# Performance work log

Hardware: AMD Instinct MI355X
Metric: run time of the kernel (lower is better)

## Reference

```python
import jax, jax.numpy as jnp
import numpy as np

D = 1024      # embed_size
H = 16        # num_heads
NEXP = 8      # num_experts
TOPK = 3
THRESH = 0.05
COEF = 0.01
B, SQ, SKV = 4, 1024, 1024


def _ln(x, g, b, eps=1e-5):
    m = jnp.mean(x, axis=-1, keepdims=True)
    v = jnp.mean(jnp.square(x - m), axis=-1, keepdims=True)
    return (x - m) * jax.lax.rsqrt(v + eps) * g + b


def setup_inputs() -> dict:
    key = jax.random.key(0)
    ks = jax.random.split(key, 20)
    s = 0.02
    w = lambda k, shape: (jax.random.normal(k, shape, jnp.float32) * s)
    return {
        'query': jax.random.normal(ks[0], (B, SQ, D), jnp.float32),
        'key_value': jax.random.normal(ks[1], (B, SKV, D), jnp.float32),
        'Wq': w(ks[2], (D, D)), 'bq': jnp.zeros((D,), jnp.float32),
        'Wk': w(ks[3], (D, D)), 'bk': jnp.zeros((D,), jnp.float32),
        'Wv': w(ks[4], (D, D)), 'bv': jnp.zeros((D,), jnp.float32),
        'W_in': w(ks[5], (3 * D, D)), 'b_in': jnp.zeros((3 * D,), jnp.float32),
        'W_out': w(ks[6], (D, D)), 'b_out': jnp.zeros((D,), jnp.float32),
        'Wa': w(ks[7], (D, D)), 'ba': jnp.zeros((D,), jnp.float32),
        'ln1_g': jnp.ones((D,), jnp.float32), 'ln1_b': jnp.zeros((D,), jnp.float32),
        'Wg': w(ks[8], (D, NEXP)),
        'ew1': w(ks[9], (NEXP, D, 4 * D)), 'eb1': jnp.zeros((NEXP, 4 * D), jnp.float32),
        'ew2': w(ks[10], (NEXP, 4 * D, D)), 'eb2': jnp.zeros((NEXP, D), jnp.float32),
        'ln2_g': jnp.ones((D,), jnp.float32), 'ln2_b': jnp.zeros((D,), jnp.float32),
    }


def reference(query, key_value, Wq, bq, Wk, bk, Wv, bv, W_in, b_in, W_out, b_out,
              Wa, ba, ln1_g, ln1_b, Wg, ew1, eb1, ew2, eb2, ln2_g, ln2_b):
    Bq, Sq, _ = query.shape
    Skv = key_value.shape[1]
    Dh = D // H
    # outer Q/K/V linears (torch Linear: x @ W.T + b)
    q = query @ Wq.T + bq
    k = key_value @ Wk.T + bk
    v = key_value @ Wv.T + bv
    # nn.MultiheadAttention in-projection
    Wiq, Wik, Wiv = jnp.split(W_in, 3, axis=0)
    biq, bik, biv = jnp.split(b_in, 3)
    qh = (q @ Wiq.T + biq).reshape(Bq, Sq, H, Dh).transpose(0, 2, 1, 3)
    kh = (k @ Wik.T + bik).reshape(Bq, Skv, H, Dh).transpose(0, 2, 1, 3)
    vh = (v @ Wiv.T + biv).reshape(Bq, Skv, H, Dh).transpose(0, 2, 1, 3)
    scores = jnp.einsum('bhqd,bhkd->bhqk', qh, kh) / jnp.sqrt(jnp.float32(Dh))
    attn = jax.nn.softmax(scores, axis=-1)
    o = jnp.einsum('bhqk,bhkd->bhqd', attn, vh).transpose(0, 2, 1, 3).reshape(Bq, Sq, D)
    o = o @ W_out.T + b_out
    # adapt + residual + first_norm
    x = _ln(o @ Wa.T + ba + query, ln1_g, ln1_b)
    # ---- MoE: top-3 softmax gating, threshold on non-top-1 gates ----
    probs = jax.nn.softmax(x @ Wg, axis=-1)                 # [B,S,E]
    topv, topi = jax.lax.top_k(probs, TOPK)                  # [B,S,3]
    keep = jnp.concatenate([jnp.ones_like(topv[..., :1], bool),
                            topv[..., 1:] >= THRESH], axis=-1)
    topv = jnp.where(keep, topv, 0.0)
    combine = jnp.sum(jax.nn.one_hot(topi, NEXP, dtype=x.dtype) * topv[..., None], axis=-2)  # [B,S,E]
    moe_out = jnp.zeros_like(x)
    for e in range(NEXP):  # small fixed expert count
        h = jax.nn.gelu(x @ ew1[e] + eb1[e], approximate=False)
        moe_out = moe_out + combine[..., e:e + 1] * (h @ ew2[e] + eb2[e])
    # load-balance aux loss: E * sum(frac_routed * mean_prob) * coef
    fe = jnp.mean((combine > 0).astype(x.dtype), axis=(0, 1))
    me = jnp.mean(probs, axis=(0, 1))
    aux = COEF * NEXP * jnp.sum(fe * me)
    out = _ln(moe_out + x, ln2_g, ln2_b)
    return out, aux
```

## Files before the change

kernel.cpp:

```cpp
#include <hip/hip_runtime.h>
#include <math.h>

#define THRESH_C 0.05f
#define COEF_C   0.01f

typedef __bf16 bf16;
typedef __bf16 bf16x8 __attribute__((ext_vector_type(8)));
typedef __bf16 bf16x4 __attribute__((ext_vector_type(4)));
typedef float  f32x4  __attribute__((ext_vector_type(4)));

__device__ __forceinline__ void ld16(void* lds_base, const void* g) {
    __builtin_amdgcn_global_load_lds(
        (const __attribute__((address_space(1))) void*)g,
        (__attribute__((address_space(3))) void*)lds_base,
        16, 0, 0);
}

__device__ __forceinline__ int xcd_swz(int orig, int nwg) {
    int q = nwg >> 3, r = nwg & 7;
    int xcd = orig & 7, idx = orig >> 3;
    return (xcd < r ? xcd * (q + 1) : r * (q + 1) + (xcd - r) * q) + idx;
}

__global__ __launch_bounds__(256) void k_f32_to_split(const float* __restrict__ in,
                                                      bf16* __restrict__ hi,
                                                      bf16* __restrict__ lo, long n) {
    long i = ((long)blockIdx.x * 256 + threadIdx.x) * 4;
    if (i >= n) return;
    float4 v = *(const float4*)(in + i);
    bf16x4 h, l;
    h[0] = (bf16)v.x; l[0] = (bf16)(v.x - (float)h[0]);
    h[1] = (bf16)v.y; l[1] = (bf16)(v.y - (float)h[1]);
    h[2] = (bf16)v.z; l[2] = (bf16)(v.z - (float)h[2]);
    h[3] = (bf16)v.w; l[3] = (bf16)(v.w - (float)h[3]);
    *(bf16x4*)(hi + i) = h;
    *(bf16x4*)(lo + i) = l;
}

__global__ __launch_bounds__(256) void k_transpose4_split(const float* __restrict__ w0,
                                                          const float* __restrict__ w1,
                                                          const float* __restrict__ w2,
                                                          const float* __restrict__ w3,
                                                          bf16* __restrict__ oh,
                                                          bf16* __restrict__ ol) {
    __shared__ float t[64][65];
    int z = blockIdx.z;
    const float* in = (z == 0) ? w0 : (z == 1) ? w1 : (z == 2) ? w2 : w3;
    bf16* ohz = oh + (long)z * 1048576;
    bf16* olz = ol + (long)z * 1048576;
    int r0 = blockIdx.y * 64, c0 = blockIdx.x * 64;
    for (int i = threadIdx.x; i < 4096; i += 256) {
        int r = i >> 6, c = i & 63;
        t[r][c] = in[(long)(r0 + r) * 1024 + (c0 + c)];
    }
    __syncthreads();
    for (int i = threadIdx.x; i < 4096; i += 256) {
        int c = i >> 6, r = i & 63;
        float v = t[r][c];
        bf16 h = (bf16)v;
        long o = (long)(c0 + c) * 1024 + (r0 + r);
        ohz[o] = h;
        olz[o] = (bf16)(v - (float)h);
    }
}

__global__ __launch_bounds__(256) void k_transpose_ew(const float* __restrict__ in,
                                                      bf16* __restrict__ out,
                                                      int R, int C) {
    __shared__ bf16 t[64][65];
    const float* ib = in + (long)blockIdx.z * R * C;
    bf16* ob = out + (long)blockIdx.z * R * C;
    int r0 = blockIdx.y * 64, c0 = blockIdx.x * 64;
    for (int i = threadIdx.x; i < 4096; i += 256) {
        int r = i >> 6, c = i & 63;
        t[r][c] = (bf16)ib[(long)(r0 + r) * C + (c0 + c)];
    }
    __syncthreads();
    for (int i = threadIdx.x; i < 4096; i += 256) {
        int c = i >> 6, r = i & 63;
        ob[(long)(c0 + c) * R + (r0 + r)] = t[r][c];
    }
}

__global__ __launch_bounds__(256) void k_bias_fold4(const float* __restrict__ W_in,
                                                    const float* __restrict__ Wa,
                                                    const float* __restrict__ bq,
                                                    const float* __restrict__ bk,
                                                    const float* __restrict__ bv,
                                                    const float* __restrict__ b_out,
                                                    const float* __restrict__ b_in,
                                                    const float* __restrict__ ba,
                                                    float* __restrict__ y) {
    int z = blockIdx.y;
    const float* W  = (z < 3) ? (W_in + (long)z * 1048576) : Wa;
    const float* b1 = (z == 0) ? bq : (z == 1) ? bk : (z == 2) ? bv : b_out;
    const float* b2 = (z < 3) ? (b_in + z * 1024) : ba;
    int row = blockIdx.x * 4 + (threadIdx.x >> 6);
    int lane = threadIdx.x & 63;
    const float* wr = W + (long)row * 1024;
    float s = 0.f;
    for (int k = lane; k < 1024; k += 64) s += wr[k] * b1[k];
#pragma unroll
    for (int o = 32; o >= 1; o >>= 1) s += __shfl_xor(s, o);
    if (lane == 0) y[z * 1024 + row] = b2[row] + s;
}

enum { HP_SPLIT = 0, HP_F32 = 1, HP_SPLIT_HEADS = 2 };

template<int MODE>
__global__ __launch_bounds__(256)
void gemm_hp(const bf16* __restrict__ Ah, const bf16* __restrict__ Al, int lda, long sAz,
             const bf16* __restrict__ Bh, const bf16* __restrict__ Bl, int ldb, long sBz,
             void* __restrict__ Chv, bf16* __restrict__ Cl, int ldc, long sCz,
             const float* __restrict__ bias, long sbz, float alpha, int M, int N, int K) {
    __shared__ alignas(16) bf16 sAh[128 * 32];
    __shared__ alignas(16) bf16 sAl[128 * 32];
    __shared__ alignas(16) bf16 sBh[128 * 32];
    __shared__ alignas(16) bf16 sBl[128 * 32];
    const int bm = blockIdx.y, bn = blockIdx.x, z = blockIdx.z;
    const int tid  = threadIdx.x;
    const int lane = tid & 63, wave = tid >> 6;
    const int quad = lane >> 4, l16 = lane & 15;
    const int wr = wave >> 1, wc = wave & 1;
    const int sr = tid >> 2;
    const int sc = (tid & 3) * 8;

    int arow0 = min(bm * 128 + sr, M - 1);
    int arow1 = min(bm * 128 + sr + 64, M - 1);
    int brow0 = min(bn * 128 + sr, N - 1);
    int brow1 = min(bn * 128 + sr + 64, N - 1);

    const bf16* pAh0 = Ah + (long)z * sAz + (long)arow0 * lda + sc;
    const bf16* pAh1 = Ah + (long)z * sAz + (long)arow1 * lda + sc;
    const bf16* pAl0 = Al + (long)z * sAz + (long)arow0 * lda + sc;
    const bf16* pAl1 = Al + (long)z * sAz + (long)arow1 * lda + sc;
    const bf16* pBh0 = Bh + (long)z * sBz + (long)brow0 * ldb + sc;
    const bf16* pBh1 = Bh + (long)z * sBz + (long)brow1 * ldb + sc;
    const bf16* pBl0 = Bl + (long)z * sBz + (long)brow0 * ldb + sc;
    const bf16* pBl1 = Bl + (long)z * sBz + (long)brow1 * ldb + sc;
    const int wo = wave << 9;

    f32x4 acc[4][4];
#pragma unroll
    for (int i = 0; i < 4; i++)
#pragma unroll
        for (int j = 0; j < 4; j++) acc[i][j] = (f32x4){0.f, 0.f, 0.f, 0.f};

    ld16(sAh + wo,        pAh0);
    ld16(sAh + 2048 + wo, pAh1);
    ld16(sAl + wo,        pAl0);
    ld16(sAl + 2048 + wo, pAl1);
    ld16(sBh + wo,        pBh0);
    ld16(sBh + 2048 + wo, pBh1);
    ld16(sBl + wo,        pBl0);
    ld16(sBl + 2048 + wo, pBl1);
    __syncthreads();

    for (int k0 = 0; k0 < K; k0 += 32) {
        bf16x8 ah[4], al[4], bh[4], bl[4];
#pragma unroll
        for (int i = 0; i < 4; i++) {
            int ro = (wr * 64 + i * 16 + l16) * 32 + quad * 8;
            ah[i] = *(const bf16x8*)&sAh[ro];
            al[i] = *(const bf16x8*)&sAl[ro];
        }
#pragma unroll
        for (int j = 0; j < 4; j++) {
            int ro = (wc * 64 + j * 16 + l16) * 32 + quad * 8;
            bh[j] = *(const bf16x8*)&sBh[ro];
            bl[j] = *(const bf16x8*)&sBl[ro];
        }
        __syncthreads();
        int kn = k0 + 32;
        if (kn < K) {
            ld16(sAh + wo,        pAh0 + kn);
            ld16(sAh + 2048 + wo, pAh1 + kn);
            ld16(sAl + wo,        pAl0 + kn);
            ld16(sAl + 2048 + wo, pAl1 + kn);
            ld16(sBh + wo,        pBh0 + kn);
            ld16(sBh + 2048 + wo, pBh1 + kn);
            ld16(sBl + wo,        pBl0 + kn);
            ld16(sBl + 2048 + wo, pBl1 + kn);
        }
#pragma unroll
        for (int i = 0; i < 4; i++)
#pragma unroll
            for (int j = 0; j < 4; j++) {
                acc[i][j] = __builtin_amdgcn_mfma_f32_16x16x32_bf16(al[i], bh[j], acc[i][j], 0, 0, 0);
                acc[i][j] = __builtin_amdgcn_mfma_f32_16x16x32_bf16(ah[i], bl[j], acc[i][j], 0, 0, 0);
                acc[i][j] = __builtin_amdgcn_mfma_f32_16x16x32_bf16(ah[i], bh[j], acc[i][j], 0, 0, 0);
            }
        __syncthreads();
    }

#pragma unroll
    for (int i = 0; i < 4; i++) {
        int mbase = bm * 128 + wr * 64 + i * 16 + quad * 4;
#pragma unroll
        for (int j = 0; j < 4; j++) {
            int n = bn * 128 + wc * 64 + j * 16 + l16;
            if (n < N) {
                float bv = bias ? bias[(long)z * sbz + n] : 0.f;
#pragma unroll
                for (int r = 0; r < 4; r++) {
                    int m = mbase + r;
                    if (m < M) {
                        float v = alpha * acc[i][j][r] + bv;
                        if (MODE == HP_SPLIT) {
                            long cidx = (long)z * sCz + (long)m * ldc + n;
                            bf16 h = (bf16)v;
                            ((bf16*)Chv)[cidx] = h;
                            Cl[cidx] = (bf16)(v - (float)h);
                        } else if (MODE == HP_F32) {
                            long cidx = (long)z * sCz + (long)m * ldc + n;
                            ((float*)Chv)[cidx] = v;
                        } else {
                            int slice = ((m >> 10) << 4) + (n >> 6);
                            long idx = (long)z * sCz + (long)slice * 65536 + (long)(m & 1023) * 64 + (n & 63);
                            bf16 h = (bf16)v;
                            ((bf16*)Chv)[idx] = h;
                            Cl[idx] = (bf16)(v - (float)h);
                        }
                    }
                }
            }
        }
    }
}

__global__ __launch_bounds__(256)
void gemm_pv(const bf16* __restrict__ Ph, const bf16* __restrict__ Pl,
             const bf16* __restrict__ Vh, const bf16* __restrict__ Vl,
             bf16* __restrict__ Oh, bf16* __restrict__ Ol) {
    __shared__ alignas(16) bf16 sAh[2][128 * 32];
    __shared__ alignas(16) bf16 sAl[2][128 * 32];
    __shared__ alignas(16) bf16 sBh[2][64 * 32];
    __shared__ alignas(16) bf16 sBl[2][64 * 32];
    const int bm = blockIdx.x, z = blockIdx.y;
    const int tid = threadIdx.x, lane = tid & 63, wave = tid >> 6;
    const int quad = lane >> 4, l16 = lane & 15;
    const int wr = wave & 1, wc = wave >> 1;
    const int sr = tid >> 2, sc = (tid & 3) * 8;

    const bf16* pA0h = Ph + (long)z * 1048576 + (long)(bm * 128 + sr) * 1024 + sc;
    const bf16* pA1h = pA0h + 64 * 1024;
    const bf16* pA0l = Pl + (long)z * 1048576 + (long)(bm * 128 + sr) * 1024 + sc;
    const bf16* pA1l = pA0l + 64 * 1024;
    const bf16* pB0h = Vh + (long)z * 65536 + (long)sr * 1024 + sc;
    const bf16* pB0l = Vl + (long)z * 65536 + (long)sr * 1024 + sc;
    const int wo = wave << 9;

    f32x4 acc[4][2];
#pragma unroll
    for (int i = 0; i < 4; i++)
#pragma unroll
        for (int j = 0; j < 2; j++) acc[i][j] = (f32x4){0.f, 0.f, 0.f, 0.f};

    ld16(sAh[0] + wo,        pA0h);
    ld16(sAh[0] + 2048 + wo, pA1h);
    ld16(sAl[0] + wo,        pA0l);
    ld16(sAl[0] + 2048 + wo, pA1l);
    ld16(sBh[0] + wo, pB0h);
    ld16(sBl[0] + wo, pB0l);
    __syncthreads();

    int cur = 0;
    for (int k0 = 0; k0 < 1024; k0 += 32) {
        int kn = k0 + 32;
        if (kn < 1024) {
            ld16(sAh[cur ^ 1] + wo,        pA0h + kn);
            ld16(sAh[cur ^ 1] + 2048 + wo, pA1h + kn);
            ld16(sAl[cur ^ 1] + wo,        pA0l + kn);
            ld16(sAl[cur ^ 1] + 2048 + wo, pA1l + kn);
            ld16(sBh[cur ^ 1] + wo, pB0h + kn);
            ld16(sBl[cur ^ 1] + wo, pB0l + kn);
        }
        const bf16* cAh = sAh[cur]; const bf16* cAl = sAl[cur];
        const bf16* cBh = sBh[cur]; const bf16* cBl = sBl[cur];
        bf16x8 ah[4], al[4], bh[2], bl[2];
#pragma unroll
        for (int i = 0; i < 4; i++) {
            int ro = (wr * 64 + i * 16 + l16) * 32 + quad * 8;
            ah[i] = *(const bf16x8*)&cAh[ro];
            al[i] = *(const bf16x8*)&cAl[ro];
        }
#pragma unroll
        for (int j = 0; j < 2; j++) {
            int ro = (wc * 32 + j * 16 + l16) * 32 + quad * 8;
            bh[j] = *(const bf16x8*)&cBh[ro];
            bl[j] = *(const bf16x8*)&cBl[ro];
        }
#pragma unroll
        for (int i = 0; i < 4; i++)
#pragma unroll
            for (int j = 0; j < 2; j++) {
                acc[i][j] = __builtin_amdgcn_mfma_f32_16x16x32_bf16(al[i], bh[j], acc[i][j], 0, 0, 0);
                acc[i][j] = __builtin_amdgcn_mfma_f32_16x16x32_bf16(ah[i], bl[j], acc[i][j], 0, 0, 0);
                acc[i][j] = __builtin_amdgcn_mfma_f32_16x16x32_bf16(ah[i], bh[j], acc[i][j], 0, 0, 0);
            }
        __syncthreads();
        cur ^= 1;
    }

#pragma unroll
    for (int i = 0; i < 4; i++) {
        int mbase = bm * 128 + wr * 64 + i * 16 + quad * 4;
#pragma unroll
        for (int j = 0; j < 2; j++) {
            int n = wc * 32 + j * 16 + l16;
#pragma unroll
            for (int r = 0; r < 4; r++) {
                int m = mbase + r;
                long idx = (long)z * 65536 + (long)m * 64 + n;
                float v = acc[i][j][r];
                bf16 h = (bf16)v;
                Oh[idx] = h;
                Ol[idx] = (bf16)(v - (float)h);
            }
        }
    }
}

__global__ __launch_bounds__(256)
void gemm_moe1(const bf16* __restrict__ Ae, const bf16* __restrict__ ew1t,
               const float* __restrict__ eb1, bf16* __restrict__ Hp,
               const int* __restrict__ counts, const int* __restrict__ bases,
               const int* __restrict__ tiles, const int* __restrict__ ntile) {
    const int wg = xcd_swz(blockIdx.x, gridDim.x);
    const int tile = wg >> 5;
    const int bn = wg & 31;
    if (tile >= ntile[0]) return;
    const int te = tiles[tile];
    const int e = te >> 16, bm = te & 0xffff;
    const int M = counts[e];
    const bf16* A = Ae + (long)bases[e] * 1024;
    const bf16* B = ew1t + (long)e * 4194304;
    bf16* C = Hp + (long)bases[e] * 4096;
    const float* bias = eb1 + e * 4096;

    __shared__ alignas(16) bf16 sA[2][128 * 32];
    __shared__ alignas(16) bf16 sB[2][128 * 32];
    const int tid  = threadIdx.x;
    const int lane = tid & 63, wave = tid >> 6;
    const int quad = lane >> 4, l16 = lane & 15;
    const int wr = wave >> 1, wc = wave & 1;
    const int sr = tid >> 2;
    const int sc = (tid & 3) * 8;

    int arow0 = min(bm * 128 + sr, M - 1);
    int arow1 = min(bm * 128 + sr + 64, M - 1);
    int brow0 = bn * 128 + sr;
    const bf16* pA0 = A + (long)arow0 * 1024 + sc;
    const bf16* pA1 = A + (long)arow1 * 1024 + sc;
    const bf16* pB0 = B + (long)brow0 * 1024 + sc;
    const bf16* pB1 = B + (long)(brow0 + 64) * 1024 + sc;
    const int wo = wave << 9;

    f32x4 acc[4][4];
#pragma unroll
    for (int i = 0; i < 4; i++)
#pragma unroll
        for (int j = 0; j < 4; j++) acc[i][j] = (f32x4){0.f, 0.f, 0.f, 0.f};

    ld16(sA[0] + wo,        pA0);
    ld16(sA[0] + 2048 + wo, pA1);
    ld16(sB[0] + wo,        pB0);
    ld16(sB[0] + 2048 + wo, pB1);
    __syncthreads();

    int cur = 0;
    for (int k0 = 0; k0 < 1024; k0 += 32) {
        int kn = k0 + 32;
        if (kn < 1024) {
            ld16(sA[cur ^ 1] + wo,        pA0 + kn);
            ld16(sA[cur ^ 1] + 2048 + wo, pA1 + kn);
            ld16(sB[cur ^ 1] + wo,        pB0 + kn);
            ld16(sB[cur ^ 1] + 2048 + wo, pB1 + kn);
        }
        const bf16* cA = sA[cur]; const bf16* cB = sB[cur];
        bf16x8 af[4], bfr[4];
#pragma unroll
        for (int i = 0; i < 4; i++)
            af[i] = *(const bf16x8*)&cA[(wr * 64 + i * 16 + l16) * 32 + quad * 8];
#pragma unroll
        for (int j = 0; j < 4; j++)
            bfr[j] = *(const bf16x8*)&cB[(wc * 64 + j * 16 + l16) * 32 + quad * 8];
#pragma unroll
        for (int i = 0; i < 4; i++)
#pragma unroll
            for (int j = 0; j < 4; j++)
                acc[i][j] = __builtin_amdgcn_mfma_f32_16x16x32_bf16(af[i], bfr[j], acc[i][j], 0, 0, 0);
        __syncthreads();
        cur ^= 1;
    }

#pragma unroll
    for (int i = 0; i < 4; i++) {
        int mbase = bm * 128 + wr * 64 + i * 16 + quad * 4;
#pragma unroll
        for (int j = 0; j < 4; j++) {
            int n = bn * 128 + wc * 64 + j * 16 + l16;
            float bv = bias[n];
#pragma unroll
            for (int r = 0; r < 4; r++) {
                int m = mbase + r;
                if (m < M) {
                    float v = acc[i][j][r] + bv;
                    float g = 0.5f * v * (1.f + erff(v * 0.70710678118654752f));
                    C[(long)m * 4096 + n] = (bf16)g;
                }
            }
        }
    }
}

__global__ __launch_bounds__(256)
void gemm_moe2(const bf16* __restrict__ Hp, const bf16* __restrict__ ew2t,
               float* __restrict__ Y,
               const int* __restrict__ counts, const int* __restrict__ bases,
               const int* __restrict__ tiles, const int* __restrict__ ntile) {
    const int wg = xcd_swz(blockIdx.x, gridDim.x);
    const int tile = wg >> 3;
    const int bn = wg & 7;
    if (tile >= ntile[0]) return;
    const int te = tiles[tile];
    const int e = te >> 16, bm = te & 0xffff;
    const int M = counts[e];
    const bf16* A = Hp + (long)bases[e] * 4096;
    const bf16* B = ew2t + (long)e * 4194304;
    float* C = Y + (long)bases[e] * 1024;

    __shared__ alignas(16) bf16 sA[2][128 * 32];
    __shared__ alignas(16) bf16 sB[2][128 * 32];
    const int tid  = threadIdx.x;
    const int lane = tid & 63, wave = tid >> 6;
    const int quad = lane >> 4, l16 = lane & 15;
    const int wr = wave >> 1, wc = wave & 1;
    const int sr = tid >> 2;
    const int sc = (tid & 3) * 8;

    int arow0 = min(bm * 128 + sr, M - 1);
    int arow1 = min(bm * 128 + sr + 64, M - 1);
    int brow0 = bn * 128 + sr;
    const bf16* pA0 = A + (long)arow0 * 4096 + sc;
    const bf16* pA1 = A + (long)arow1 * 4096 + sc;
    const bf16* pB0 = B + (long)brow0 * 4096 + sc;
    const bf16* pB1 = B + (long)(brow0 + 64) * 4096 + sc;
    const int wo = wave << 9;

    f32x4 acc[4][4];
#pragma unroll
    for (int i = 0; i < 4; i++)
#pragma unroll
        for (int j = 0; j < 4; j++) acc[i][j] = (f32x4){0.f, 0.f, 0.f, 0.f};

    ld16(sA[0] + wo,        pA0);
    ld16(sA[0] + 2048 + wo, pA1);
    ld16(sB[0] + wo,        pB0);
    ld16(sB[0] + 2048 + wo, pB1);
    __syncthreads();

    int cur = 0;
    for (int k0 = 0; k0 < 4096; k0 += 32) {
        int kn = k0 + 32;
        if (kn < 4096) {
            ld16(sA[cur ^ 1] + wo,        pA0 + kn);
            ld16(sA[cur ^ 1] + 2048 + wo, pA1 + kn);
            ld16(sB[cur ^ 1] + wo,        pB0 + kn);
            ld16(sB[cur ^ 1] + 2048 + wo, pB1 + kn);
        }
        const bf16* cA = sA[cur]; const bf16* cB = sB[cur];
        bf16x8 af[4], bfr[4];
#pragma unroll
        for (int i = 0; i < 4; i++)
            af[i] = *(const bf16x8*)&cA[(wr * 64 + i * 16 + l16) * 32 + quad * 8];
#pragma unroll
        for (int j = 0; j < 4; j++)
            bfr[j] = *(const bf16x8*)&cB[(wc * 64 + j * 16 + l16) * 32 + quad * 8];
#pragma unroll
        for (int i = 0; i < 4; i++)
#pragma unroll
            for (int j = 0; j < 4; j++)
                acc[i][j] = __builtin_amdgcn_mfma_f32_16x16x32_bf16(af[i], bfr[j], acc[i][j], 0, 0, 0);
        __syncthreads();
        cur ^= 1;
    }

#pragma unroll
    for (int i = 0; i < 4; i++) {
        int mbase = bm * 128 + wr * 64 + i * 16 + quad * 4;
#pragma unroll
        for (int j = 0; j < 4; j++) {
            int n = bn * 128 + wc * 64 + j * 16 + l16;
#pragma unroll
            for (int r = 0; r < 4; r++) {
                int m = mbase + r;
                if (m < M) C[(long)m * 1024 + n] = acc[i][j][r];
            }
        }
    }
}

__global__ __launch_bounds__(256) void k_vsplit(const bf16* __restrict__ VH_h,
                                                const bf16* __restrict__ VH_l,
                                                bf16* __restrict__ VT_h,
                                                bf16* __restrict__ VT_l) {
    __shared__ bf16 th[64][65];
    __shared__ bf16 tl[64][65];
    int s = blockIdx.y, q0 = blockIdx.x * 64;
    int b = s >> 4, h = s & 15;
    long ibase = ((long)(b * 1024 + q0)) * 1024 + h * 64;
    for (int i = threadIdx.x; i < 4096; i += 256) {
        int q = i >> 6, d = i & 63;
        th[q][d] = VH_h[ibase + (long)q * 1024 + d];
        tl[q][d] = VH_l[ibase + (long)q * 1024 + d];
    }
    __syncthreads();
    long obase = (long)s * 65536 + q0;
    for (int i = threadIdx.x; i < 4096; i += 256) {
        int d = i >> 6, q = i & 63;
        VT_h[obase + (long)d * 1024 + q] = th[q][d];
        VT_l[obase + (long)d * 1024 + q] = tl[q][d];
    }
}

__global__ __launch_bounds__(256) void k_ocopy(const bf16* __restrict__ Op_h,
                                               const bf16* __restrict__ Op_l,
                                               bf16* __restrict__ O_h,
                                               bf16* __restrict__ O_l) {
    int t = blockIdx.x * 4 + (threadIdx.x >> 6);
    int lane = threadIdx.x & 63;
    int b = t >> 10, q = t & 1023;
    int h = lane >> 2, dd = (lane & 3) * 16;
    long src = ((long)(b * 16 + h)) * 65536 + (long)q * 64 + dd;
    long dst = (long)t * 1024 + h * 64 + dd;
    *(bf16x8*)(O_h + dst)     = *(const bf16x8*)(Op_h + src);
    *(bf16x8*)(O_h + dst + 8) = *(const bf16x8*)(Op_h + src + 8);
    *(bf16x8*)(O_l + dst)     = *(const bf16x8*)(Op_l + src);
    *(bf16x8*)(O_l + dst + 8) = *(const bf16x8*)(Op_l + src + 8);
}

__global__ __launch_bounds__(256) void k_gather(const bf16* __restrict__ Xb,
                                                const int* __restrict__ tok,
                                                const int* __restrict__ counts,
                                                const int* __restrict__ bases,
                                                bf16* __restrict__ Ae) {
    int e = blockIdx.y;
    int cnt = counts[e];
    long base = bases[e];
    for (int i = blockIdx.x; i < cnt; i += gridDim.x) {
        int t = tok[e * 4096 + i];
        const bf16x4* src = (const bf16x4*)(Xb + (long)t * 1024);
        bf16x4* dst = (bf16x4*)(Ae + (base + i) * 1024);
        dst[threadIdx.x] = src[threadIdx.x];
    }
}

__global__ __launch_bounds__(256) void k_softmax_ip(bf16* __restrict__ Sh,
                                                    bf16* __restrict__ Sl) {
    int row = blockIdx.x * 4 + (threadIdx.x >> 6);
    int lane = threadIdx.x & 63;
    long o = (long)row * 1024 + lane * 16;
    bf16x8 h0 = *(const bf16x8*)(Sh + o), h1 = *(const bf16x8*)(Sh + o + 8);
    bf16x8 l0 = *(const bf16x8*)(Sl + o), l1 = *(const bf16x8*)(Sl + o + 8);
    float v[16];
#pragma unroll
    for (int i = 0; i < 8; i++) {
        v[i] = (float)h0[i] + (float)l0[i];
        v[8 + i] = (float)h1[i] + (float)l1[i];
    }
    float mx = v[0];
#pragma unroll
    for (int i = 1; i < 16; i++) mx = fmaxf(mx, v[i]);
#pragma unroll
    for (int of = 32; of >= 1; of >>= 1) mx = fmaxf(mx, __shfl_xor(mx, of));
    float s = 0.f;
#pragma unroll
    for (int i = 0; i < 16; i++) { v[i] = expf(v[i] - mx); s += v[i]; }
#pragma unroll
    for (int of = 32; of >= 1; of >>= 1) s += __shfl_xor(s, of);
    float inv = 1.f / s;
#pragma unroll
    for (int i = 0; i < 8; i++) {
        float a = v[i] * inv;
        h0[i] = (bf16)a; l0[i] = (bf16)(a - (float)h0[i]);
        float b = v[8 + i] * inv;
        h1[i] = (bf16)b; l1[i] = (bf16)(b - (float)h1[i]);
    }
    *(bf16x8*)(Sh + o) = h0;  *(bf16x8*)(Sh + o + 8) = h1;
    *(bf16x8*)(Sl + o) = l0;  *(bf16x8*)(Sl + o + 8) = l1;
}

__global__ __launch_bounds__(256) void k_ln(const float* __restrict__ xin,
                                            const float* __restrict__ resid,
                                            const float* __restrict__ g,
                                            const float* __restrict__ bb,
                                            float* __restrict__ outf,
                                            bf16* __restrict__ outb) {
    int row = blockIdx.x * 4 + (threadIdx.x >> 6);
    int lane = threadIdx.x & 63;
    long base = (long)row * 1024 + lane * 16;
    float v[16];
#pragma unroll
    for (int i = 0; i < 16; i += 4) {
        f32x4 a = *(const f32x4*)(xin + base + i);
        if (resid) { f32x4 r4 = *(const f32x4*)(resid + base + i); a += r4; }
        v[i] = a[0]; v[i + 1] = a[1]; v[i + 2] = a[2]; v[i + 3] = a[3];
    }
    float s = 0.f;
#pragma unroll
    for (int i = 0; i < 16; i++) s += v[i];
#pragma unroll
    for (int o = 32; o >= 1; o >>= 1) s += __shfl_xor(s, o);
    float mean = s * (1.f / 1024.f);
    float vs = 0.f;
#pragma unroll
    for (int i = 0; i < 16; i++) { float d = v[i] - mean; vs += d * d; }
#pragma unroll
    for (int o = 32; o >= 1; o >>= 1) vs += __shfl_xor(vs, o);
    float inv = 1.f / sqrtf(vs * (1.f / 1024.f) + 1e-5f);
    const float* gp = g + lane * 16;
    const float* bp = bb + lane * 16;
#pragma unroll
    for (int i = 0; i < 16; i++) {
        float o = (v[i] - mean) * inv * gp[i] + bp[i];
        if (outf) outf[base + i] = o;
        if (outb) outb[base + i] = (bf16)o;
    }
}

__global__ __launch_bounds__(256) void k_moe_ln(const float* __restrict__ Y,
                                                const int* __restrict__ pos,
                                                const float* __restrict__ combine,
                                                const float* __restrict__ eb2,
                                                const float* __restrict__ resid,
                                                const float* __restrict__ g,
                                                const float* __restrict__ bb,
                                                float* __restrict__ outf) {
    int row = blockIdx.x * 4 + (threadIdx.x >> 6);
    int lane = threadIdx.x & 63;
    long base = (long)row * 1024 + lane * 16;
    float v[16];
#pragma unroll
    for (int i = 0; i < 16; i += 4) {
        f32x4 a = *(const f32x4*)(resid + base + i);
        v[i] = a[0]; v[i + 1] = a[1]; v[i + 2] = a[2]; v[i + 3] = a[3];
    }
    for (int e = 0; e < 8; e++) {
        int p = pos[row * 8 + e];
        if (p >= 0) {
            float c = combine[row * 8 + e];
            const float* yr = Y + (long)p * 1024 + lane * 16;
            const float* br = eb2 + e * 1024 + lane * 16;
#pragma unroll
            for (int i = 0; i < 16; i += 4) {
                f32x4 y4 = *(const f32x4*)(yr + i);
                f32x4 b4 = *(const f32x4*)(br + i);
                v[i]     += c * (y4[0] + b4[0]);
                v[i + 1] += c * (y4[1] + b4[1]);
                v[i + 2] += c * (y4[2] + b4[2]);
                v[i + 3] += c * (y4[3] + b4[3]);
            }
        }
    }
    float s = 0.f;
#pragma unroll
    for (int i = 0; i < 16; i++) s += v[i];
#pragma unroll
    for (int o = 32; o >= 1; o >>= 1) s += __shfl_xor(s, o);
    float mean = s * (1.f / 1024.f);
    float vs = 0.f;
#pragma unroll
    for (int i = 0; i < 16; i++) { float d = v[i] - mean; vs += d * d; }
#pragma unroll
    for (int o = 32; o >= 1; o >>= 1) vs += __shfl_xor(vs, o);
    float inv = 1.f / sqrtf(vs * (1.f / 1024.f) + 1e-5f);
    const float* gp = g + lane * 16;
    const float* bp = bb + lane * 16;
#pragma unroll
    for (int i = 0; i < 16; i++)
        outf[base + i] = (v[i] - mean) * inv * gp[i] + bp[i];
}

__global__ __launch_bounds__(256) void k_gate(const float* __restrict__ X,
                                              const float* __restrict__ Wg,
                                              float* __restrict__ combine,
                                              float* __restrict__ partials) {
    __shared__ float sm[16];
    if (threadIdx.x < 16) sm[threadIdx.x] = 0.f;
    __syncthreads();
    int t = blockIdx.x * 4 + (threadIdx.x >> 6);
    int lane = threadIdx.x & 63;
    const float* x = X + (long)t * 1024;
    float acc[8] = {0.f, 0.f, 0.f, 0.f, 0.f, 0.f, 0.f, 0.f};
    for (int i = lane; i < 1024; i += 64) {
        float xv = x[i];
        const float* w = Wg + i * 8;
#pragma unroll
        for (int e = 0; e < 8; e++) acc[e] += xv * w[e];
    }
#pragma unroll
    for (int e = 0; e < 8; e++)
#pragma unroll
        for (int o = 32; o >= 1; o >>= 1) acc[e] += __shfl_xor(acc[e], o);
    if (lane == 0) {
        float mx = acc[0];
#pragma unroll
        for (int e = 1; e < 8; e++) mx = fmaxf(mx, acc[e]);
        float p[8], s = 0.f;
#pragma unroll
        for (int e = 0; e < 8; e++) { p[e] = expf(acc[e] - mx); s += p[e]; }
        float invs = 1.f / s;
#pragma unroll
        for (int e = 0; e < 8; e++) p[e] *= invs;
        float b1 = -1.f, b2 = -1.f, b3 = -1.f; int i1 = 0, i2 = 0, i3 = 0;
#pragma unroll
        for (int e = 0; e < 8; e++) {
            float pe = p[e];
            if (pe > b1)      { b3 = b2; i3 = i2; b2 = b1; i2 = i1; b1 = pe; i1 = e; }
            else if (pe > b2) { b3 = b2; i3 = i2; b2 = pe; i2 = e; }
            else if (pe > b3) { b3 = pe; i3 = e; }
        }
        float c[8] = {0.f, 0.f, 0.f, 0.f, 0.f, 0.f, 0.f, 0.f};
        c[i1] = b1;
        if (b2 >= THRESH_C) c[i2] = b2;
        if (b3 >= THRESH_C) c[i3] = b3;
        float* co = combine + (long)t * 8;
#pragma unroll
        for (int e = 0; e < 8; e++) co[e] = c[e];
#pragma unroll
        for (int e = 0; e < 8; e++) {
            atomicAdd(&sm[e], p[e]);
            if (c[e] > 0.f) atomicAdd(&sm[8 + e], 1.f);
        }
    }
    __syncthreads();
    if (threadIdx.x < 16) partials[(long)blockIdx.x * 16 + threadIdx.x] = sm[threadIdx.x];
}

__global__ __launch_bounds__(256) void k_route(const float* __restrict__ combine,
                                               int* __restrict__ counts,
                                               int* __restrict__ bases,
                                               int* __restrict__ tok,
                                               int* __restrict__ pos,
                                               int* __restrict__ tiles,
                                               int* __restrict__ ntile) {
    __shared__ int scan[256];
    int tid = threadIdx.x;
    int mybase = 0;
    int nt = 0;
    for (int e = 0; e < 8; e++) {
        int pred[16]; int cnt = 0;
#pragma unroll
        for (int j = 0; j < 16; j++) {
            int t = tid * 16 + j;
            pred[j] = combine[t * 8 + e] > 0.f ? 1 : 0;
            cnt += pred[j];
        }
        scan[tid] = cnt;
        __syncthreads();
        for (int off = 1; off < 256; off <<= 1) {
            int v = (tid >= off) ? scan[tid - off] : 0;
            __syncthreads();
            scan[tid] += v;
            __syncthreads();
        }
        int start = scan[tid] - cnt;
        int total = scan[255];
        int o = e * 4096 + start;
        int gp = mybase + start;
#pragma unroll
        for (int j = 0; j < 16; j++) {
            int t = tid * 16 + j;
            if (pred[j]) { tok[o++] = t; pos[t * 8 + e] = gp++; }
            else pos[t * 8 + e] = -1;
        }
        if (tid == 0) {
            counts[e] = total; bases[e] = mybase;
            int nte = (total + 127) >> 7;
            for (int b = 0; b < nte; b++) tiles[nt++] = (e << 16) | b;
        }
        mybase += total;
        __syncthreads();
    }
    if (tid == 0) ntile[0] = nt;
}

__global__ __launch_bounds__(256) void k_aux(const float* __restrict__ partials, int nblocks,
                                             float* __restrict__ auxout) {
    __shared__ float red[256];
    int tid = threadIdx.x;
    int e = tid & 15, grp = tid >> 4;
    float s = 0.f;
    for (int b = grp; b < nblocks; b += 16) s += partials[(long)b * 16 + e];
    red[tid] = s;
    __syncthreads();
    if (grp == 0) {
        float tot = 0.f;
        for (int g2 = 0; g2 < 16; g2++) tot += red[g2 * 16 + e];
        red[tid] = tot;
    }
    __syncthreads();
    if (tid == 0) {
        float s2 = 0.f;
        for (int e2 = 0; e2 < 8; e2++)
            s2 += (red[8 + e2] * (1.f / 4096.f)) * (red[e2] * (1.f / 4096.f));
        auxout[0] = COEF_C * 8.f * s2;
    }
}

extern "C" void kernel_launch(void* const* d_in, const int* in_sizes, int n_in,
                              void* d_out, int out_size, void* d_ws, size_t ws_size,
                              hipStream_t stream) {
    const float* query     = (const float*)d_in[0];
    const float* key_value = (const float*)d_in[1];
    const float* Wq   = (const float*)d_in[2];
    const float* bq   = (const float*)d_in[3];
    const float* Wk   = (const float*)d_in[4];
    const float* bk   = (const float*)d_in[5];
    const float* Wv   = (const float*)d_in[6];
    const float* bv   = (const float*)d_in[7];
    const float* W_in = (const float*)d_in[8];
    const float* b_in = (const float*)d_in[9];
    const float* W_out = (const float*)d_in[10];
    const float* b_out = (const float*)d_in[11];
    const float* Wa   = (const float*)d_in[12];
    const float* ba   = (const float*)d_in[13];
    const float* ln1_g = (const float*)d_in[14];
    const float* ln1_b = (const float*)d_in[15];
    const float* Wg   = (const float*)d_in[16];
    const float* ew1  = (const float*)d_in[17];
    const float* eb1  = (const float*)d_in[18];
    const float* ew2  = (const float*)d_in[19];
    const float* eb2  = (const float*)d_in[20];
    const float* ln2_g = (const float*)d_in[21];
    const float* ln2_b = (const float*)d_in[22];

    const size_t MBY = 1ull << 20;
    const long MB1 = 1024L * 1024L;
    char* ws = (char*)d_ws;

    bf16* Sh   = (bf16*)(ws + 0 * MBY);
    bf16* Sl   = (bf16*)(ws + 64 * MBY);
    bf16* ew1t = (bf16*)(ws + 0 * MBY);
    bf16* ew2t = (bf16*)(ws + 64 * MBY);
    bf16* WAll_h = (bf16*)(ws + 128 * MBY);
    bf16* WAll_l = (bf16*)(ws + 136 * MBY);
    bf16* WT_h   = (bf16*)(ws + 144 * MBY);
    bf16* WT_l   = (bf16*)(ws + 152 * MBY);
    bf16* Xq_h  = (bf16*)(ws + 160 * MBY), *Xq_l  = (bf16*)(ws + 168 * MBY);
    bf16* Xkv_h = (bf16*)(ws + 176 * MBY), *Xkv_l = (bf16*)(ws + 184 * MBY);
    bf16* O_h  = (bf16*)(ws + 160 * MBY), *O_l  = (bf16*)(ws + 168 * MBY);
    bf16* QHp_h = (bf16*)(ws + 192 * MBY), *QHp_l = (bf16*)(ws + 200 * MBY);
    bf16* KHp_h = (bf16*)(ws + 208 * MBY), *KHp_l = (bf16*)(ws + 216 * MBY);
    bf16* VH_h  = (bf16*)(ws + 224 * MBY), *VH_l  = (bf16*)(ws + 232 * MBY);
    bf16* VTp_h = (bf16*)(ws + 240 * MBY), *VTp_l = (bf16*)(ws + 248 * MBY);
    bf16* Op_h  = (bf16*)(ws + 256 * MBY), *Op_l  = (bf16*)(ws + 264 * MBY);
    float* Xf   = (float*)(ws + 256 * MBY);
    float* Af   = (float*)(ws + 272 * MBY);
    bf16* Ae      = (bf16*)(ws + 128 * MBY);
    bf16* Hp      = (bf16*)(ws + 152 * MBY);
    float* Yp     = (float*)(ws + 272 * MBY);
    bf16* Xb   = (bf16*)(ws + 320 * MBY);
    bf16* Weff_h = (bf16*)(ws + 328 * MBY);
    bf16* Weff_l = (bf16*)(ws + 336 * MBY);
    float* combine  = (float*)(ws + 344 * MBY);
    float* partials = (float*)(ws + 344 * MBY + 128 * 1024);
    float* beff     = (float*)(ws + 344 * MBY + 192 * 1024);
    int*   counts   = (int*)  (ws + 344 * MBY + 212 * 1024);
    int*   bases    = (int*)  (ws + 344 * MBY + 213 * 1024);
    int*   tok      = (int*)  (ws + 344 * MBY + 214 * 1024);
    int*   pos      = (int*)  (ws + 344 * MBY + 342 * 1024);
    int*   tiles    = (int*)  (ws + 344 * MBY + 472 * 1024);
    int*   ntile    = tiles + 128;

    dim3 blk(256);

    k_f32_to_split<<<4096, blk, 0, stream>>>(query, Xq_h, Xq_l, 4L * MB1);
    k_f32_to_split<<<4096, blk, 0, stream>>>(key_value, Xkv_h, Xkv_l, 4L * MB1);
    k_f32_to_split<<<3072, blk, 0, stream>>>(W_in, WAll_h, WAll_l, 3L * MB1);
    k_f32_to_split<<<1024, blk, 0, stream>>>(Wa, WAll_h + 3 * MB1, WAll_l + 3 * MB1, MB1);
    k_transpose4_split<<<dim3(16, 16, 4), blk, 0, stream>>>(Wq, Wk, Wv, W_out, WT_h, WT_l);
    k_bias_fold4<<<dim3(256, 4), blk, 0, stream>>>(W_in, Wa, bq, bk, bv, b_out, b_in, ba, beff);

    gemm_hp<HP_SPLIT><<<dim3(8, 8, 4), blk, 0, stream>>>(
        WAll_h, WAll_l, 1024, MB1, WT_h, WT_l, 1024, MB1,
        Weff_h, Weff_l, 1024, MB1, nullptr, 0, 1.f, 1024, 1024, 1024);

    gemm_hp<HP_SPLIT_HEADS><<<dim3(8, 32, 2), blk, 0, stream>>>(
        Xq_h, Xq_l, 1024, 8 * MB1, Weff_h, Weff_l, 1024, MB1,
        QHp_h, QHp_l, 0, 8 * MB1, beff, 1024, 1.f, 4096, 1024, 1024);
    gemm_hp<HP_SPLIT><<<dim3(8, 32, 1), blk, 0, stream>>>(
        Xkv_h, Xkv_l, 1024, 0, Weff_h + 2 * MB1, Weff_l + 2 * MB1, 1024, 0,
        VH_h, VH_l, 1024, 0, beff + 2048, 0, 1.f, 4096, 1024, 1024);
    k_vsplit<<<dim3(16, 64), blk, 0, stream>>>(VH_h, VH_l, VTp_h, VTp_l);

    for (int half = 0; half < 2; half++) {
        long so = (long)half * 32 * 65536;
        gemm_hp<HP_SPLIT><<<dim3(8, 8, 32), blk, 0, stream>>>(
            QHp_h + so, QHp_l + so, 64, 65536,
            KHp_h + so, KHp_l + so, 64, 65536,
            Sh, Sl, 1024, MB1, nullptr, 0, 0.125f, 1024, 1024, 64);
        k_softmax_ip<<<8192, blk, 0, stream>>>(Sh, Sl);
        gemm_pv<<<dim3(8, 32), blk, 0, stream>>>(Sh, Sl, VTp_h + so, VTp_l + so,
                                                 Op_h + so, Op_l + so);
    }
    k_ocopy<<<1024, blk, 0, stream>>>(Op_h, Op_l, O_h, O_l);

    gemm_hp<HP_F32><<<dim3(8, 32, 1), blk, 0, stream>>>(
        O_h, O_l, 1024, 0, Weff_h + 3 * MB1, Weff_l + 3 * MB1, 1024, 0,
        Af, nullptr, 1024, 0, beff + 3072, 0, 1.f, 4096, 1024, 1024);
    k_ln<<<1024, blk, 0, stream>>>(Af, query, ln1_g, ln1_b, Xf, Xb);
    k_gate<<<1024, blk, 0, stream>>>(Xf, Wg, combine, partials);
    k_route<<<1, blk, 0, stream>>>(combine, counts, bases, tok, pos, tiles, ntile);
    k_gather<<<dim3(512, 8), blk, 0, stream>>>(Xb, tok, counts, bases, Ae);

    k_transpose_ew<<<dim3(64, 16, 8), blk, 0, stream>>>(ew1, ew1t, 1024, 4096);
    k_transpose_ew<<<dim3(16, 64, 8), blk, 0, stream>>>(ew2, ew2t, 4096, 1024);

    gemm_moe1<<<dim3(104 * 32), blk, 0, stream>>>(Ae, ew1t, eb1, Hp, counts, bases, tiles, ntile);
    gemm_moe2<<<dim3(104 * 8), blk, 0, stream>>>(Hp, ew2t, Yp, counts, bases, tiles, ntile);

    k_moe_ln<<<1024, blk, 0, stream>>>(Yp, pos, combine, eb2, Xf, ln2_g, ln2_b, (float*)d_out);
    k_aux<<<1, blk, 0, stream>>>(partials, 1024, (float*)d_out + (out_size - 1));
}
```

Before: 1.552 ms.

## Merge QKV projection launches, parallelize routing per expert, single-buffer MoE GEMMs

Merges the Q/K and V projection GEMMs into one launch with a new output mode: z<2 writes the head-split layout and z=2 writes row-major V. Splits the single-block routing kernel into one block per expert plus a small finalize kernel that computes bases and the tile list, so pos now holds per-expert offsets that k_moe_ln adds to bases[e]. Also drops double buffering in the MoE GEMMs in favour of a single LDS buffer with two barriers per k-step. This cuts launch count and serial routing work, but the global loads in the MoE GEMMs can no longer overlap with the MFMA work.

```diff
diff --git a/kernel.cpp b/kernel.cpp
--- a/kernel.cpp
+++ b/kernel.cpp
@@ -105,7 +105,7 @@
     if (lane == 0) y[z * 1024 + row] = b2[row] + s;
 }
 
-enum { HP_SPLIT = 0, HP_F32 = 1, HP_SPLIT_HEADS = 2 };
+enum { HP_SPLIT = 0, HP_F32 = 1, HP_SPLIT_HEADS = 2, HP_PROJ_QKV = 3 };
 
 template<int MODE>
 __global__ __launch_bounds__(256)
@@ -130,10 +130,11 @@
     int brow0 = min(bn * 128 + sr, N - 1);
     int brow1 = min(bn * 128 + sr + 64, N - 1);
 
-    const bf16* pAh0 = Ah + (long)z * sAz + (long)arow0 * lda + sc;
-    const bf16* pAh1 = Ah + (long)z * sAz + (long)arow1 * lda + sc;
-    const bf16* pAl0 = Al + (long)z * sAz + (long)arow0 * lda + sc;
-    const bf16* pAl1 = Al + (long)z * sAz + (long)arow1 * lda + sc;
+    const long zA = (MODE == HP_PROJ_QKV) ? (long)min(z, 1) : (long)z;
+    const bf16* pAh0 = Ah + zA * sAz + (long)arow0 * lda + sc;
+    const bf16* pAh1 = Ah + zA * sAz + (long)arow1 * lda + sc;
+    const bf16* pAl0 = Al + zA * sAz + (long)arow0 * lda + sc;
+    const bf16* pAl1 = Al + zA * sAz + (long)arow1 * lda + sc;
     const bf16* pBh0 = Bh + (long)z * sBz + (long)brow0 * ldb + sc;
     const bf16* pBh1 = Bh + (long)z * sBz + (long)brow1 * ldb + sc;
     const bf16* pBl0 = Bl + (long)z * sBz + (long)brow0 * ldb + sc;
@@ -214,9 +215,20 @@
                         } else if (MODE == HP_F32) {
                             long cidx = (long)z * sCz + (long)m * ldc + n;
                             ((float*)Chv)[cidx] = v;
-                        } else {
+                        } else if (MODE == HP_SPLIT_HEADS) {
                             int slice = ((m >> 10) << 4) + (n >> 6);
                             long idx = (long)z * sCz + (long)slice * 65536 + (long)(m & 1023) * 64 + (n & 63);
+                            bf16 h = (bf16)v;
+                            ((bf16*)Chv)[idx] = h;
+                            Cl[idx] = (bf16)(v - (float)h);
+                        } else {
+                            long idx;
+                            if (z < 2) {
+                                int slice = ((m >> 10) << 4) + (n >> 6);
+                                idx = (long)z * sCz + (long)slice * 65536 + (long)(m & 1023) * 64 + (n & 63);
+                            } else {
+                                idx = (long)z * sCz + (long)m * ldc + n;
+                            }
                             bf16 h = (bf16)v;
                             ((bf16*)Chv)[idx] = h;
                             Cl[idx] = (bf16)(v - (float)h);
@@ -338,8 +350,8 @@
     bf16* C = Hp + (long)bases[e] * 4096;
     const float* bias = eb1 + e * 4096;
 
-    __shared__ alignas(16) bf16 sA[2][128 * 32];
-    __shared__ alignas(16) bf16 sB[2][128 * 32];
+    __shared__ alignas(16) bf16 sA[128 * 32];
+    __shared__ alignas(16) bf16 sB[128 * 32];
     const int tid  = threadIdx.x;
     const int lane = tid & 63, wave = tid >> 6;
     const int quad = lane >> 4, l16 = lane & 15;
@@ -362,36 +374,25 @@
 #pragma unroll
         for (int j = 0; j < 4; j++) acc[i][j] = (f32x4){0.f, 0.f, 0.f, 0.f};
 
-    ld16(sA[0] + wo,        pA0);
-    ld16(sA[0] + 2048 + wo, pA1);
-    ld16(sB[0] + wo,        pB0);
-    ld16(sB[0] + 2048 + wo, pB1);
-    __syncthreads();
-
-    int cur = 0;
     for (int k0 = 0; k0 < 1024; k0 += 32) {
-        int kn = k0 + 32;
-        if (kn < 1024) {
-            ld16(sA[cur ^ 1] + wo,        pA0 + kn);
-            ld16(sA[cur ^ 1] + 2048 + wo, pA1 + kn);
-            ld16(sB[cur ^ 1] + wo,        pB0 + kn);
-            ld16(sB[cur ^ 1] + 2048 + wo, pB1 + kn);
-        }
-        const bf16* cA = sA[cur]; const bf16* cB = sB[cur];
+        __syncthreads();
+        ld16(sA + wo,        pA0 + k0);
+        ld16(sA + 2048 + wo, pA1 + k0);
+        ld16(sB + wo,        pB0 + k0);
+        ld16(sB + 2048 + wo, pB1 + k0);
+        __syncthreads();
         bf16x8 af[4], bfr[4];
 #pragma unroll
         for (int i = 0; i < 4; i++)
-            af[i] = *(const bf16x8*)&cA[(wr * 64 + i * 16 + l16) * 32 + quad * 8];
+            af[i] = *(const bf16x8*)&sA[(wr * 64 + i * 16 + l16) * 32 + quad * 8];
 #pragma unroll
         for (int j = 0; j < 4; j++)
-            bfr[j] = *(const bf16x8*)&cB[(wc * 64 + j * 16 + l16) * 32 + quad * 8];
+            bfr[j] = *(const bf16x8*)&sB[(wc * 64 + j * 16 + l16) * 32 + quad * 8];
 #pragma unroll
         for (int i = 0; i < 4; i++)
 #pragma unroll
             for (int j = 0; j < 4; j++)
                 acc[i][j] = __builtin_amdgcn_mfma_f32_16x16x32_bf16(af[i], bfr[j], acc[i][j], 0, 0, 0);
-        __syncthreads();
-        cur ^= 1;
     }
 
 #pragma unroll
@@ -430,8 +431,8 @@
     const bf16* B = ew2t + (long)e * 4194304;
     float* C = Y + (long)bases[e] * 1024;
 
-    __shared__ alignas(16) bf16 sA[2][128 * 32];
-    __shared__ alignas(16) bf16 sB[2][128 * 32];
+    __shared__ alignas(16) bf16 sA[128 * 32];
+    __shared__ alignas(16) bf16 sB[128 * 32];
     const int tid  = threadIdx.x;
     const int lane = tid & 63, wave = tid >> 6;
     const int quad = lane >> 4, l16 = lane & 15;
@@ -454,36 +455,25 @@
 #pragma unroll
         for (int j = 0; j < 4; j++) acc[i][j] = (f32x4){0.f, 0.f, 0.f, 0.f};
 
-    ld16(sA[0] + wo,        pA0);
-    ld16(sA[0] + 2048 + wo, pA1);
-    ld16(sB[0] + wo,        pB0);
-    ld16(sB[0] + 2048 + wo, pB1);
-    __syncthreads();
-
-    int cur = 0;
     for (int k0 = 0; k0 < 4096; k0 += 32) {
-        int kn = k0 + 32;
-        if (kn < 4096) {
-            ld16(sA[cur ^ 1] + wo,        pA0 + kn);
-            ld16(sA[cur ^ 1] + 2048 + wo, pA1 + kn);
-            ld16(sB[cur ^ 1] + wo,        pB0 + kn);
-            ld16(sB[cur ^ 1] + 2048 + wo, pB1 + kn);
-        }
-        const bf16* cA = sA[cur]; const bf16* cB = sB[cur];
+        __syncthreads();
+        ld16(sA + wo,        pA0 + k0);
+        ld16(sA + 2048 + wo, pA1 + k0);
+        ld16(sB + wo,        pB0 + k0);
+        ld16(sB + 2048 + wo, pB1 + k0);
+        __syncthreads();
         bf16x8 af[4], bfr[4];
 #pragma unroll
         for (int i = 0; i < 4; i++)
-            af[i] = *(const bf16x8*)&cA[(wr * 64 + i * 16 + l16) * 32 + quad * 8];
+            af[i] = *(const bf16x8*)&sA[(wr * 64 + i * 16 + l16) * 32 + quad * 8];
 #pragma unroll
         for (int j = 0; j < 4; j++)
-            bfr[j] = *(const bf16x8*)&cB[(wc * 64 + j * 16 + l16) * 32 + quad * 8];
+            bfr[j] = *(const bf16x8*)&sB[(wc * 64 + j * 16 + l16) * 32 + quad * 8];
 #pragma unroll
         for (int i = 0; i < 4; i++)
 #pragma unroll
             for (int j = 0; j < 4; j++)
                 acc[i][j] = __builtin_amdgcn_mfma_f32_16x16x32_bf16(af[i], bfr[j], acc[i][j], 0, 0, 0);
-        __syncthreads();
-        cur ^= 1;
     }
 
 #pragma unroll
@@ -631,6 +621,7 @@
 
 __global__ __launch_bounds__(256) void k_moe_ln(const float* __restrict__ Y,
                                                 const int* __restrict__ pos,
+                                                const int* __restrict__ bases,
                                                 const float* __restrict__ combine,
                                                 const float* __restrict__ eb2,
                                                 const float* __restrict__ resid,
@@ -650,7 +641,7 @@
         int p = pos[row * 8 + e];
         if (p >= 0) {
             float c = combine[row * 8 + e];
-            const float* yr = Y + (long)p * 1024 + lane * 16;
+            const float* yr = Y + (long)(bases[e] + p) * 1024 + lane * 16;
             const float* br = eb2 + e * 1024 + lane * 16;
 #pragma unroll
             for (int i = 0; i < 16; i += 4) {
@@ -738,52 +729,54 @@
     if (threadIdx.x < 16) partials[(long)blockIdx.x * 16 + threadIdx.x] = sm[threadIdx.x];
 }
 
-__global__ __launch_bounds__(256) void k_route(const float* __restrict__ combine,
-                                               int* __restrict__ counts,
-                                               int* __restrict__ bases,
-                                               int* __restrict__ tok,
-                                               int* __restrict__ pos,
-                                               int* __restrict__ tiles,
-                                               int* __restrict__ ntile) {
+__global__ __launch_bounds__(256) void k_route_e(const float* __restrict__ combine,
+                                                 int* __restrict__ counts,
+                                                 int* __restrict__ tok,
+                                                 int* __restrict__ pos) {
     __shared__ int scan[256];
+    int e = blockIdx.x;
     int tid = threadIdx.x;
-    int mybase = 0;
-    int nt = 0;
-    for (int e = 0; e < 8; e++) {
-        int pred[16]; int cnt = 0;
-#pragma unroll
-        for (int j = 0; j < 16; j++) {
-            int t = tid * 16 + j;
-            pred[j] = combine[t * 8 + e] > 0.f ? 1 : 0;
-            cnt += pred[j];
-        }
-        scan[tid] = cnt;
+    int pred[16]; int cnt = 0;
+#pragma unroll
+    for (int j = 0; j < 16; j++) {
+        int t = tid * 16 + j;
+        pred[j] = combine[t * 8 + e] > 0.f ? 1 : 0;
+        cnt += pred[j];
+    }
+    scan[tid] = cnt;
+    __syncthreads();
+    for (int off = 1; off < 256; off <<= 1) {
+        int v = (tid >= off) ? scan[tid - off] : 0;
         __syncthreads();
-        for (int off = 1; off < 256; off <<= 1) {
-            int v = (tid >= off) ? scan[tid - off] : 0;
-            __syncthreads();
-            scan[tid] += v;
-            __syncthreads();
-        }
-        int start = scan[tid] - cnt;
-        int total = scan[255];
-        int o = e * 4096 + start;
-        int gp = mybase + start;
-#pragma unroll
-        for (int j = 0; j < 16; j++) {
-            int t = tid * 16 + j;
-            if (pred[j]) { tok[o++] = t; pos[t * 8 + e] = gp++; }
-            else pos[t * 8 + e] = -1;
-        }
-        if (tid == 0) {
-            counts[e] = total; bases[e] = mybase;
-            int nte = (total + 127) >> 7;
-            for (int b = 0; b < nte; b++) tiles[nt++] = (e << 16) | b;
-        }
-        mybase += total;
+        scan[tid] += v;
         __syncthreads();
     }
-    if (tid == 0) ntile[0] = nt;
+    int start = scan[tid] - cnt;
+    int o = e * 4096 + start;
+    int gp = start;
+#pragma unroll
+    for (int j = 0; j < 16; j++) {
+        int t = tid * 16 + j;
+        if (pred[j]) { tok[o++] = t; pos[t * 8 + e] = gp++; }
+        else pos[t * 8 + e] = -1;
+    }
+    if (tid == 0) counts[e] = scan[255];
+}
+
+__global__ __launch_bounds__(64) void k_route_fin(const int* __restrict__ counts,
+                                                  int* __restrict__ bases,
+                                                  int* __restrict__ tiles,
+                                                  int* __restrict__ ntile) {
+    if (threadIdx.x == 0) {
+        int b = 0, nt = 0;
+        for (int e = 0; e < 8; e++) {
+            bases[e] = b;
+            int nte = (counts[e] + 127) >> 7;
+            for (int bb = 0; bb < nte; bb++) tiles[nt++] = (e << 16) | bb;
+            b += counts[e];
+        }
+        ntile[0] = nt;
+    }
 }
 
 __global__ __launch_bounds__(256) void k_aux(const float* __restrict__ partials, int nblocks,
@@ -887,12 +880,9 @@
         WAll_h, WAll_l, 1024, MB1, WT_h, WT_l, 1024, MB1,
         Weff_h, Weff_l, 1024, MB1, nullptr, 0, 1.f, 1024, 1024, 1024);
 
-    gemm_hp<HP_SPLIT_HEADS><<<dim3(8, 32, 2), blk, 0, stream>>>(
+    gemm_hp<HP_PROJ_QKV><<<dim3(8, 32, 3), blk, 0, stream>>>(
         Xq_h, Xq_l, 1024, 8 * MB1, Weff_h, Weff_l, 1024, MB1,
-        QHp_h, QHp_l, 0, 8 * MB1, beff, 1024, 1.f, 4096, 1024, 1024);
-    gemm_hp<HP_SPLIT><<<dim3(8, 32, 1), blk, 0, stream>>>(
-        Xkv_h, Xkv_l, 1024, 0, Weff_h + 2 * MB1, Weff_l + 2 * MB1, 1024, 0,
-        VH_h, VH_l, 1024, 0, beff + 2048, 0, 1.f, 4096, 1024, 1024);
+        QHp_h, QHp_l, 1024, 8 * MB1, beff, 1024, 1.f, 4096, 1024, 1024);
     k_vsplit<<<dim3(16, 64), blk, 0, stream>>>(VH_h, VH_l, VTp_h, VTp_l);
 
     for (int half = 0; half < 2; half++) {
@@ -912,7 +902,8 @@
         Af, nullptr, 1024, 0, beff + 3072, 0, 1.f, 4096, 1024, 1024);
     k_ln<<<1024, blk, 0, stream>>>(Af, query, ln1_g, ln1_b, Xf, Xb);
     k_gate<<<1024, blk, 0, stream>>>(Xf, Wg, combine, partials);
-    k_route<<<1, blk, 0, stream>>>(combine, counts, bases, tok, pos, tiles, ntile);
+    k_route_e<<<8, blk, 0, stream>>>(combine, counts, tok, pos);
+    k_route_fin<<<1, 64, 0, stream>>>(counts, bases, tiles, ntile);
     k_gather<<<dim3(512, 8), blk, 0, stream>>>(Xb, tok, counts, bases, Ae);
 
     k_transpose_ew<<<dim3(64, 16, 8), blk, 0, stream>>>(ew1, ew1t, 1024, 4096);
@@ -921,6 +912,6 @@
     gemm_moe1<<<dim3(104 * 32), blk, 0, stream>>>(Ae, ew1t, eb1, Hp, counts, bases, tiles, ntile);
     gemm_moe2<<<dim3(104 * 8), blk, 0, stream>>>(Hp, ew2t, Yp, counts, bases, tiles, ntile);
 
-    k_moe_ln<<<1024, blk, 0, stream>>>(Yp, pos, combine, eb2, Xf, ln2_g, ln2_b, (float*)d_out);
+    k_moe_ln<<<1024, blk, 0, stream>>>(Yp, pos, bases, combine, eb2, Xf, ln2_g, ln2_b, (float*)d_out);
     k_aux<<<1, blk, 0, stream>>>(partials, 1024, (float*)d_out + (out_size - 1));
 }
```

After: 1.458 ms. -6.0%, faster.
